# Kernel tuning notes

Measured on AMD Instinct MI355X. Metric: run time of the kernel, lower is better.

Reference implementation:

```python
import jax, jax.numpy as jnp
import numpy as np

NUM_NODES = 32768  # B*N = 16*2048
NUM_REL = 10
NUM_BASES = 4
D = 256
E = 524288


def _rgcn_layer(x, src, dst, rel, basis, comp, root, bias):
    """Basis-decomposed relational GCN layer with per-relation mean aggregation.
    x: [N, Din], basis: [NB, Din, Dout], comp: [R, NB], root: [Din, Dout], bias: [Dout].
    """
    n = x.shape[0]
    # project all nodes through each basis once: [N, NB, Dout]
    xb = jnp.einsum('ni,bio->nbo', x, basis)
    coeff = comp[rel]  # [E, NB] per-edge basis coefficients
    # mean normalization per (destination node, relation) pair
    seg = rel * n + dst  # combined segment id, [E]
    cnt = jax.ops.segment_sum(jnp.ones(rel.shape[0], x.dtype), seg,
                              num_segments=NUM_REL * n)
    inv = jnp.where(cnt > 0, 1.0 / cnt, 0.0)[seg]  # [E]
    # per-edge message: sum_b coeff[e,b] * xb[src_e, b, :] (loop over small NB)
    msg = jnp.zeros((rel.shape[0], basis.shape[2]), x.dtype)
    for b in range(basis.shape[0]):
        msg = msg + coeff[:, b:b + 1] * xb[src, b]
    msg = msg * inv[:, None]
    agg = jax.ops.segment_sum(msg, dst, num_segments=n)  # [N, Dout]
    return agg + x @ root + bias


def setup_inputs() -> dict:
    key = jax.random.key(0)
    ks = jax.random.split(key, 16)
    p = lambda k, shp: (jax.random.normal(k, shp, jnp.float32) * 0.05)
    inp = {
        'x': jax.random.normal(ks[0], (16, 2048, D), jnp.float32),
        't': jax.random.randint(ks[1], (16,), 0, 1000),
        'obj_cond': jax.random.randint(ks[2], (16, 2048), 0, 160),
        'edge_cond': jax.random.randint(ks[3], (2, E), 0, NUM_NODES),
        'relation_cond': jax.random.randint(ks[4], (E,), 0, NUM_REL),
        # layer 0: 256 -> 256 (hidden)
        'basis0': p(ks[5], (NUM_BASES, D, D)),
        'comp0': p(ks[6], (NUM_REL, NUM_BASES)),
        'root0': p(ks[7], (D, D)),
        'bias0': p(ks[8], (D,)),
        # layer 1: 256 -> 256 (output)
        'basis1': p(ks[9], (NUM_BASES, D, D)),
        'comp1': p(ks[10], (NUM_REL, NUM_BASES)),
        'root1': p(ks[11], (D, D)),
        'bias1': p(ks[12], (D,)),
    }
    return inp


def reference(x, t, obj_cond, edge_cond, relation_cond,
              basis0, comp0, root0, bias0, basis1, comp1, root1, bias1):
    B, N, Dm = x.shape
    h = x.reshape(B * N, Dm)
    src, dst = edge_cond[0], edge_cond[1]
    h = _rgcn_layer(h, src, dst, relation_cond, basis0, comp0, root0, bias0)
    h = jax.nn.relu(h)  # hidden-layer activation (dropout disabled at eval)
    h = _rgcn_layer(h, src, dst, relation_cond, basis1, comp1, root1, bias1)
    return h.reshape(B, N, Dm)
```

## Files before the change

kernel.cpp:

```cpp
#include <hip/hip_runtime.h>
#include <stdint.h>

#define NNODES 32768
#define NREL 10
#define NBASES 4
#define DIM 256
#define NEDGE 524288
#define KW 1280
#define KBASE 1024

#define HB 2048
#define CB 8192
#define WB 80

typedef __attribute__((ext_vector_type(8))) short bf16x8;
typedef __attribute__((ext_vector_type(4))) float f32x4;
typedef __attribute__((ext_vector_type(2))) float f32x2;

__device__ __forceinline__ float bf2f(unsigned short u){
  union { unsigned int i; float f; } v; v.i = ((unsigned int)u) << 16; return v.f;
}
__device__ __forceinline__ float asf(unsigned int u){
  union { unsigned int i; float f; } v; v.i = u; return v.f;
}
__device__ __forceinline__ unsigned short f2bf(float f){
  union { float f; unsigned int i; } v; v.f = f;
  unsigned int x = v.i;
  unsigned int r = (x + 0x7FFFu + ((x >> 16) & 1u)) >> 16;
  return (unsigned short)r;
}
__device__ __forceinline__ void gll16(const void* g, void* l){
  __builtin_amdgcn_global_load_lds((const __attribute__((address_space(1))) void*)g,
                                   (__attribute__((address_space(3))) void*)l, 16, 0, 0);
}

__global__ __launch_bounds__(256) void mega_prep(
    const int* __restrict__ ec, const int* __restrict__ rel,
    int* __restrict__ cnt_rd,
    const float* __restrict__ x, unsigned short* __restrict__ Xh,
    const float* __restrict__ basis0, const float* __restrict__ root0,
    unsigned short* __restrict__ Wt0,
    const float* __restrict__ basis1, const float* __restrict__ root1,
    unsigned short* __restrict__ Wt1)
{
  __shared__ float tile[64][65];
  int bid = blockIdx.x;
  int t = threadIdx.x;
  if (bid < HB){
    int e = bid * 256 + t;
    int d = ec[NEDGE + e];
    int r = rel[e];
    atomicAdd(&cnt_rd[(r << 15) + d], 1);
  } else if (bid < HB + CB){
    int i = (bid - HB) * 256 + t;
    float4 v = ((const float4*)x)[i];
    ushort4 o; o.x = f2bf(v.x); o.y = f2bf(v.y); o.z = f2bf(v.z); o.w = f2bf(v.w);
    ((ushort4*)Xh)[i] = o;
  } else {
    int b = bid - HB - CB;
    int layer = b / WB; b %= WB;
    const float* basis = layer ? basis1 : basis0;
    const float* root  = layer ? root1  : root0;
    unsigned short* Wt = layer ? Wt1    : Wt0;
    int k0 = (b % 20) * 64;
    int n0 = (b / 20) * 64;
    int tn = t & 63, tk = t >> 6;
#pragma unroll
    for (int i = 0; i < 64; i += 4){
      int k = k0 + tk + i;
      float v = (k < KBASE) ? basis[(size_t)k * 256 + n0 + tn]
                            : root[(size_t)(k - KBASE) * 256 + n0 + tn];
      tile[tk + i][tn] = v;
    }
    __syncthreads();
#pragma unroll
    for (int i = 0; i < 64; i += 4){
      int n = n0 + tk + i;
      Wt[(size_t)n * KW + k0 + tn] = f2bf(tile[tn][tk + i]);
    }
  }
}

__global__ __launch_bounds__(1024) void scan1(const int* __restrict__ cnt_rd,
                                              int* __restrict__ offs, int* __restrict__ blksum)
{
  __shared__ int sh[1024];
  int tid = threadIdx.x; int gid = blockIdx.x * 1024 + tid;
  int v = 0;
#pragma unroll
  for (int r = 0; r < NREL; r++) v += cnt_rd[(r << 15) + gid];
  sh[tid] = v; __syncthreads();
  for (int off = 1; off < 1024; off <<= 1){
    int t = (tid >= off) ? sh[tid - off] : 0;
    __syncthreads(); sh[tid] += t; __syncthreads();
  }
  offs[gid] = sh[tid] - v;
  if (tid == 1023) blksum[blockIdx.x] = sh[1023];
}
__global__ __launch_bounds__(1024) void scan3b(int* __restrict__ offs, const int* __restrict__ blksum)
{
  __shared__ int pre;
  int bid = blockIdx.x;
  if (threadIdx.x < 64){
    int v = ((int)threadIdx.x < bid && threadIdx.x < 32) ? blksum[threadIdx.x] : 0;
#pragma unroll
    for (int o = 1; o < 64; o <<= 1) v += __shfl_xor(v, o);
    if (threadIdx.x == 0) pre = v;
  }
  __syncthreads();
  int gid = bid * 1024 + threadIdx.x;
  offs[gid] += pre;
  if (gid == 0) offs[NNODES] = NEDGE;
}

__global__ void scatter_kernel(const int* __restrict__ ec, const int* __restrict__ rel,
                               const int* __restrict__ offs, int* __restrict__ cursor,
                               unsigned int* __restrict__ meta)
{
  int e = blockIdx.x * 256 + threadIdx.x;
  int s = ec[e];
  int d = ec[NEDGE + e];
  int r = rel[e];
  int p = offs[d] + atomicAdd(&cursor[d], 1);
  meta[p] = ((unsigned int)s << 4) | (unsigned int)r;
}

__global__ __launch_bounds__(256) void agg8(
    const unsigned short* __restrict__ Xin,
    const int* __restrict__ offs,
    const unsigned int* __restrict__ meta,
    const float* __restrict__ comp,
    const int* __restrict__ cnt_rd,
    unsigned short* __restrict__ z)
{
  __shared__ __attribute__((aligned(16))) float wtab[4][40];
  int t = threadIdx.x;
  int wv = t >> 6, lane = t & 63;
  int d = blockIdx.x * 4 + wv;
  if (lane < 40){
    int r = lane >> 2, b = lane & 3;
    int cnt = cnt_rd[(r << 15) + d];
    wtab[wv][lane] = (cnt > 0) ? comp[r * NBASES + b] / (float)cnt : 0.0f;
  }
  __syncthreads();

  const float4* wt4 = (const float4*)&wtab[wv][0];
  const char* Xb = (const char*)Xin;
  unsigned colb = (unsigned)(lane * 8);

  f32x2 acc[NBASES][2];
#pragma unroll
  for (int b = 0; b < NBASES; b++){ acc[b][0] = (f32x2){0.f,0.f}; acc[b][1] = (f32x2){0.f,0.f}; }

  int e0 = offs[d], e1 = offs[d + 1];
  int e = e0;

  for (; e + 7 < e1; e += 8){
    unsigned int m[8];
#pragma unroll
    for (int i = 0; i < 8; i++) m[i] = meta[e + i];
    uint2 v[8];
#pragma unroll
    for (int i = 0; i < 8; i++){
      unsigned off = ((m[i] & 0xFFFFFFF0u) << 5) + colb;
      v[i] = *(const uint2*)(Xb + off);
    }
#pragma unroll
    for (int i = 0; i < 8; i++){
      float4 w = wt4[m[i] & 15u];
      f32x2 f01, f23;
      f01.x = asf(v[i].x << 16); f01.y = asf(v[i].x & 0xffff0000u);
      f23.x = asf(v[i].y << 16); f23.y = asf(v[i].y & 0xffff0000u);
      acc[0][0] += (f32x2){w.x, w.x} * f01;  acc[0][1] += (f32x2){w.x, w.x} * f23;
      acc[1][0] += (f32x2){w.y, w.y} * f01;  acc[1][1] += (f32x2){w.y, w.y} * f23;
      acc[2][0] += (f32x2){w.z, w.z} * f01;  acc[2][1] += (f32x2){w.z, w.z} * f23;
      acc[3][0] += (f32x2){w.w, w.w} * f01;  acc[3][1] += (f32x2){w.w, w.w} * f23;
    }
  }

  for (; e < e1; e += 4){
    unsigned int m[4];
    float4 w[4];
#pragma unroll
    for (int i = 0; i < 4; i++){
      int ei = e + i;
      bool ok = ei < e1;
      m[i] = meta[ok ? ei : e1 - 1];
      float4 ww = wt4[m[i] & 15u];
      if (!ok){ ww.x = 0.f; ww.y = 0.f; ww.z = 0.f; ww.w = 0.f; }
      w[i] = ww;
    }
    uint2 v[4];
#pragma unroll
    for (int i = 0; i < 4; i++){
      unsigned off = ((m[i] & 0xFFFFFFF0u) << 5) + colb;
      v[i] = *(const uint2*)(Xb + off);
    }
#pragma unroll
    for (int i = 0; i < 4; i++){
      f32x2 f01, f23;
      f01.x = asf(v[i].x << 16); f01.y = asf(v[i].x & 0xffff0000u);
      f23.x = asf(v[i].y << 16); f23.y = asf(v[i].y & 0xffff0000u);
      acc[0][0] += (f32x2){w[i].x, w[i].x} * f01;  acc[0][1] += (f32x2){w[i].x, w[i].x} * f23;
      acc[1][0] += (f32x2){w[i].y, w[i].y} * f01;  acc[1][1] += (f32x2){w[i].y, w[i].y} * f23;
      acc[2][0] += (f32x2){w[i].z, w[i].z} * f01;  acc[2][1] += (f32x2){w[i].z, w[i].z} * f23;
      acc[3][0] += (f32x2){w[i].w, w[i].w} * f01;  acc[3][1] += (f32x2){w[i].w, w[i].w} * f23;
    }
  }

#pragma unroll
  for (int b = 0; b < NBASES; b++){
    ushort4 o;
    o.x = f2bf(acc[b][0].x); o.y = f2bf(acc[b][0].y);
    o.z = f2bf(acc[b][1].x); o.w = f2bf(acc[b][1].y);
    *(ushort4*)(z + (size_t)d * KBASE + b * 256 + lane * 4) = o;
  }
}

__global__ __launch_bounds__(256) void gemm8(
    const unsigned short* __restrict__ A0,
    const unsigned short* __restrict__ A1,
    const unsigned short* __restrict__ Wt,
    const float* __restrict__ bias,
    unsigned short* __restrict__ outh,
    float* __restrict__ outf,
    int mode)
{
  __shared__ __attribute__((aligned(16))) short As[64 * 64];
  int tid  = threadIdx.x;
  int m0   = blockIdx.x * 64;
  int lane = tid & 63;
  int wn   = tid >> 6;
  int lq = lane >> 4, lr = lane & 15;

  f32x4 zero = {0.f, 0.f, 0.f, 0.f};
  f32x4 acc[4][4];
#pragma unroll
  for (int i = 0; i < 4; i++)
#pragma unroll
    for (int j = 0; j < 4; j++) acc[i][j] = zero;

  int arow0 = tid >> 3;
  int akc0  = ((tid & 7) - (tid >> 4)) & 7;
  int g1    = tid + 256;
  int arow1 = g1 >> 3;
  int akc1  = ((g1 & 7) - (g1 >> 4)) & 7;

  const unsigned short* wtb[4];
#pragma unroll
  for (int j = 0; j < 4; j++)
    wtb[j] = Wt + (size_t)(wn * 64 + j * 16 + lr) * KW + lq * 8;

  for (int k0 = 0; k0 < KW; k0 += 64){
    __syncthreads();
    {
      const unsigned short* ga0, *ga1;
      if (k0 < KBASE){
        ga0 = A0 + (size_t)(m0 + arow0) * KBASE + k0 + akc0 * 8;
        ga1 = A0 + (size_t)(m0 + arow1) * KBASE + k0 + akc1 * 8;
      } else {
        ga0 = A1 + (size_t)(m0 + arow0) * 256 + (k0 - KBASE) + akc0 * 8;
        ga1 = A1 + (size_t)(m0 + arow1) * 256 + (k0 - KBASE) + akc1 * 8;
      }
      gll16(ga0, As + tid * 8);
      gll16(ga1, As + (tid + 256) * 8);
    }
    bf16x8 bfr[4][2];
#pragma unroll
    for (int j = 0; j < 4; j++)
#pragma unroll
      for (int s = 0; s < 2; s++)
        bfr[j][s] = *(const bf16x8*)(wtb[j] + k0 + s * 32);
    __syncthreads();

    bf16x8 af[4][2];
#pragma unroll
    for (int i = 0; i < 4; i++){
      int row = i * 16 + lr;
#pragma unroll
      for (int s = 0; s < 2; s++){
        int slot = ((lq + 4 * s) + (row >> 1)) & 7;
        af[i][s] = *(const bf16x8*)(As + row * 64 + slot * 8);
      }
    }
#pragma unroll
    for (int i = 0; i < 4; i++)
#pragma unroll
      for (int j = 0; j < 4; j++){
        acc[i][j] = __builtin_amdgcn_mfma_f32_16x16x32_bf16(af[i][0], bfr[j][0], acc[i][j], 0, 0, 0);
        acc[i][j] = __builtin_amdgcn_mfma_f32_16x16x32_bf16(af[i][1], bfr[j][1], acc[i][j], 0, 0, 0);
      }
  }

#pragma unroll
  for (int i = 0; i < 4; i++)
#pragma unroll
    for (int j = 0; j < 4; j++)
#pragma unroll
      for (int r = 0; r < 4; r++){
        int gm = m0 + i * 16 + lq * 4 + r;
        int gn = wn * 64 + j * 16 + lr;
        float v = acc[i][j][r] + bias[gn];
        size_t idx = (size_t)gm * 256 + gn;
        if (mode == 1) outh[idx] = f2bf(fmaxf(v, 0.f));
        else           outf[idx] = v;
      }
}

extern "C" void kernel_launch(void* const* d_in, const int* in_sizes, int n_in,
                              void* d_out, int out_size, void* d_ws, size_t ws_size,
                              hipStream_t stream)
{
  const float* x      = (const float*)d_in[0];
  const int*   ec     = (const int*)d_in[3];
  const int*   rel    = (const int*)d_in[4];
  const float* basis0 = (const float*)d_in[5];
  const float* comp0  = (const float*)d_in[6];
  const float* root0  = (const float*)d_in[7];
  const float* bias0  = (const float*)d_in[8];
  const float* basis1 = (const float*)d_in[9];
  const float* comp1  = (const float*)d_in[10];
  const float* root1  = (const float*)d_in[11];
  const float* bias1  = (const float*)d_in[12];

  char* p = (char*)d_ws;
  unsigned short* z   = (unsigned short*)p; p += (size_t)NNODES * KBASE * 2;
  unsigned short* Xh  = (unsigned short*)p; p += (size_t)NNODES * DIM * 2;
  unsigned short* h   = (unsigned short*)p; p += (size_t)NNODES * DIM * 2;
  unsigned short* Wt0 = (unsigned short*)p; p += (size_t)256 * KW * 2;
  unsigned short* Wt1 = (unsigned short*)p; p += (size_t)256 * KW * 2;
  unsigned int* meta  = (unsigned int*)p;   p += (size_t)NEDGE * 4;
  int* cnt_rd  = (int*)p;   p += (size_t)NREL * NNODES * 4;
  int* cursor  = (int*)p;   p += (size_t)NNODES * 4;
  int* offs    = (int*)p;   p += (size_t)(NNODES + 1) * 4;
  int* blksum  = (int*)p;   p += 1024;

  hipMemsetAsync(cnt_rd, 0, ((size_t)NREL * NNODES + (size_t)NNODES) * 4, stream);

  mega_prep<<<HB + CB + 2 * WB, 256, 0, stream>>>(
      ec, rel, cnt_rd, x, Xh, basis0, root0, Wt0, basis1, root1, Wt1);

  scan1<<<NNODES / 1024, 1024, 0, stream>>>(cnt_rd, offs, blksum);
  scan3b<<<NNODES / 1024, 1024, 0, stream>>>(offs, blksum);
  scatter_kernel<<<NEDGE / 256, 256, 0, stream>>>(ec, rel, offs, cursor, meta);

  agg8<<<NNODES / 4, 256, 0, stream>>>(Xh, offs, meta, comp0, cnt_rd, z);
  gemm8<<<NNODES / 64, 256, 0, stream>>>(z, Xh, Wt0, bias0, h, nullptr, 1);

  agg8<<<NNODES / 4, 256, 0, stream>>>(h, offs, meta, comp1, cnt_rd, z);
  gemm8<<<NNODES / 64, 256, 0, stream>>>(z, h, Wt1, bias1, nullptr, (float*)d_out, 2);
}
```

Measured before the change: 352.0 us.

## Retile GEMM to 128x128 with LDS-staged weights; simplify scan and CSR scatter

The GEMM moves from 64-row tiles that read weights straight from global into registers to 128x128 output tiles. Both A and B are staged in LDS with 32-wide K steps and a 2x2 wave layout, which raises data reuse per block. The scan now uses wavefront shuffles instead of a barrier-heavy shared-memory Hillis-Steele loop. The scatter step increments the offsets array in place, so the separate cursor buffer and part of the memset are gone, and the aggregation reads [offs[d-1], offs[d]). The tradeoffs are fewer blocks (512), twice as many K iterations with barriers, and offsets that now rely on in-place atomics.

```diff
diff --git a/kernel.cpp b/kernel.cpp
--- a/kernel.cpp
+++ b/kernel.cpp
@@ -84,18 +84,33 @@
 __global__ __launch_bounds__(1024) void scan1(const int* __restrict__ cnt_rd,
                                               int* __restrict__ offs, int* __restrict__ blksum)
 {
-  __shared__ int sh[1024];
+  __shared__ int wsum[16];
   int tid = threadIdx.x; int gid = blockIdx.x * 1024 + tid;
+  int lane = tid & 63, wv = tid >> 6;
   int v = 0;
 #pragma unroll
   for (int r = 0; r < NREL; r++) v += cnt_rd[(r << 15) + gid];
-  sh[tid] = v; __syncthreads();
-  for (int off = 1; off < 1024; off <<= 1){
-    int t = (tid >= off) ? sh[tid - off] : 0;
-    __syncthreads(); sh[tid] += t; __syncthreads();
-  }
-  offs[gid] = sh[tid] - v;
-  if (tid == 1023) blksum[blockIdx.x] = sh[1023];
+  int incl = v;
+#pragma unroll
+  for (int o = 1; o < 64; o <<= 1){
+    int t = __shfl_up(incl, o);
+    if (lane >= o) incl += t;
+  }
+  if (lane == 63) wsum[wv] = incl;
+  __syncthreads();
+  if (wv == 0){
+    int s = (lane < 16) ? wsum[lane] : 0;
+#pragma unroll
+    for (int o = 1; o < 16; o <<= 1){
+      int t = __shfl_up(s, o);
+      if (lane >= o) s += t;
+    }
+    if (lane < 16) wsum[lane] = s;
+  }
+  __syncthreads();
+  int base = wv ? wsum[wv - 1] : 0;
+  offs[gid] = base + incl - v;
+  if (tid == 1023) blksum[blockIdx.x] = base + incl;
 }
 __global__ __launch_bounds__(1024) void scan3b(int* __restrict__ offs, const int* __restrict__ blksum)
 {
@@ -110,18 +125,17 @@
   __syncthreads();
   int gid = bid * 1024 + threadIdx.x;
   offs[gid] += pre;
-  if (gid == 0) offs[NNODES] = NEDGE;
 }
 
 __global__ void scatter_kernel(const int* __restrict__ ec, const int* __restrict__ rel,
-                               const int* __restrict__ offs, int* __restrict__ cursor,
+                               int* __restrict__ offs,
                                unsigned int* __restrict__ meta)
 {
   int e = blockIdx.x * 256 + threadIdx.x;
   int s = ec[e];
   int d = ec[NEDGE + e];
   int r = rel[e];
-  int p = offs[d] + atomicAdd(&cursor[d], 1);
+  int p = atomicAdd(&offs[d], 1);
   meta[p] = ((unsigned int)s << 4) | (unsigned int)r;
 }
 
@@ -152,7 +166,8 @@
 #pragma unroll
   for (int b = 0; b < NBASES; b++){ acc[b][0] = (f32x2){0.f,0.f}; acc[b][1] = (f32x2){0.f,0.f}; }
 
-  int e0 = offs[d], e1 = offs[d + 1];
+  int e1 = offs[d];
+  int e0 = (d == 0) ? 0 : offs[d - 1];
   int e = e0;
 
   for (; e + 7 < e1; e += 8){
@@ -217,7 +232,7 @@
   }
 }
 
-__global__ __launch_bounds__(256) void gemm8(
+__global__ __launch_bounds__(256) void gemm9(
     const unsigned short* __restrict__ A0,
     const unsigned short* __restrict__ A1,
     const unsigned short* __restrict__ Wt,
@@ -226,11 +241,15 @@
     float* __restrict__ outf,
     int mode)
 {
-  __shared__ __attribute__((aligned(16))) short As[64 * 64];
+  __shared__ __attribute__((aligned(16))) short As[128 * 32];
+  __shared__ __attribute__((aligned(16))) short Bs[128 * 32];
   int tid  = threadIdx.x;
-  int m0   = blockIdx.x * 64;
+  int bid  = blockIdx.x;
+  int m0   = (bid >> 1) * 128;
+  int n0   = (bid & 1) * 128;
   int lane = tid & 63;
-  int wn   = tid >> 6;
+  int w    = tid >> 6;
+  int wm   = w >> 1, wn = w & 1;
   int lq = lane >> 4, lr = lane & 15;
 
   f32x4 zero = {0.f, 0.f, 0.f, 0.f};
@@ -240,66 +259,54 @@
 #pragma unroll
     for (int j = 0; j < 4; j++) acc[i][j] = zero;
 
-  int arow0 = tid >> 3;
-  int akc0  = ((tid & 7) - (tid >> 4)) & 7;
-  int g1    = tid + 256;
-  int arow1 = g1 >> 3;
-  int akc1  = ((g1 & 7) - (g1 >> 4)) & 7;
-
-  const unsigned short* wtb[4];
-#pragma unroll
-  for (int j = 0; j < 4; j++)
-    wtb[j] = Wt + (size_t)(wn * 64 + j * 16 + lr) * KW + lq * 8;
-
-  for (int k0 = 0; k0 < KW; k0 += 64){
+  int g1   = tid + 256;
+  int ar0  = tid >> 2, ak0 = ((tid & 3) - (tid >> 3)) & 3;
+  int ar1  = g1 >> 2,  ak1 = ((g1 & 3) - (g1 >> 3)) & 3;
+
+  for (int k0 = 0; k0 < KW; k0 += 32){
     __syncthreads();
     {
-      const unsigned short* ga0, *ga1;
+      const unsigned short *ga0, *ga1;
       if (k0 < KBASE){
-        ga0 = A0 + (size_t)(m0 + arow0) * KBASE + k0 + akc0 * 8;
-        ga1 = A0 + (size_t)(m0 + arow1) * KBASE + k0 + akc1 * 8;
+        ga0 = A0 + (size_t)(m0 + ar0) * KBASE + k0 + ak0 * 8;
+        ga1 = A0 + (size_t)(m0 + ar1) * KBASE + k0 + ak1 * 8;
       } else {
-        ga0 = A1 + (size_t)(m0 + arow0) * 256 + (k0 - KBASE) + akc0 * 8;
-        ga1 = A1 + (size_t)(m0 + arow1) * 256 + (k0 - KBASE) + akc1 * 8;
+        ga0 = A1 + (size_t)(m0 + ar0) * 256 + (k0 - KBASE) + ak0 * 8;
+        ga1 = A1 + (size_t)(m0 + ar1) * 256 + (k0 - KBASE) + ak1 * 8;
       }
       gll16(ga0, As + tid * 8);
-      gll16(ga1, As + (tid + 256) * 8);
-    }
-    bf16x8 bfr[4][2];
+      gll16(ga1, As + g1 * 8);
+      gll16(Wt + (size_t)(n0 + ar0) * KW + k0 + ak0 * 8, Bs + tid * 8);
+      gll16(Wt + (size_t)(n0 + ar1) * KW + k0 + ak1 * 8, Bs + g1 * 8);
+    }
+    __syncthreads();
+
+    bf16x8 af[4], bfr[4];
+#pragma unroll
+    for (int i = 0; i < 4; i++){
+      int row = wm * 64 + i * 16 + lr;
+      af[i] = *(const bf16x8*)(As + row * 32 + (((lq + (row >> 1)) & 3) * 8));
+    }
+#pragma unroll
+    for (int j = 0; j < 4; j++){
+      int row = wn * 64 + j * 16 + lr;
+      bfr[j] = *(const bf16x8*)(Bs + row * 32 + (((lq + (row >> 1)) & 3) * 8));
+    }
+#pragma unroll
+    for (int i = 0; i < 4; i++)
+#pragma unroll
+      for (int j = 0; j < 4; j++)
+        acc[i][j] = __builtin_amdgcn_mfma_f32_16x16x32_bf16(af[i], bfr[j], acc[i][j], 0, 0, 0);
+  }
+
+#pragma unroll
+  for (int i = 0; i < 4; i++)
 #pragma unroll
     for (int j = 0; j < 4; j++)
 #pragma unroll
-      for (int s = 0; s < 2; s++)
-        bfr[j][s] = *(const bf16x8*)(wtb[j] + k0 + s * 32);
-    __syncthreads();
-
-    bf16x8 af[4][2];
-#pragma unroll
-    for (int i = 0; i < 4; i++){
-      int row = i * 16 + lr;
-#pragma unroll
-      for (int s = 0; s < 2; s++){
-        int slot = ((lq + 4 * s) + (row >> 1)) & 7;
-        af[i][s] = *(const bf16x8*)(As + row * 64 + slot * 8);
-      }
-    }
-#pragma unroll
-    for (int i = 0; i < 4; i++)
-#pragma unroll
-      for (int j = 0; j < 4; j++){
-        acc[i][j] = __builtin_amdgcn_mfma_f32_16x16x32_bf16(af[i][0], bfr[j][0], acc[i][j], 0, 0, 0);
-        acc[i][j] = __builtin_amdgcn_mfma_f32_16x16x32_bf16(af[i][1], bfr[j][1], acc[i][j], 0, 0, 0);
-      }
-  }
-
-#pragma unroll
-  for (int i = 0; i < 4; i++)
-#pragma unroll
-    for (int j = 0; j < 4; j++)
-#pragma unroll
       for (int r = 0; r < 4; r++){
-        int gm = m0 + i * 16 + lq * 4 + r;
-        int gn = wn * 64 + j * 16 + lr;
+        int gm = m0 + wm * 64 + i * 16 + lq * 4 + r;
+        int gn = n0 + wn * 64 + j * 16 + lr;
         float v = acc[i][j][r] + bias[gn];
         size_t idx = (size_t)gm * 256 + gn;
         if (mode == 1) outh[idx] = f2bf(fmaxf(v, 0.f));
@@ -331,22 +338,21 @@
   unsigned short* Wt1 = (unsigned short*)p; p += (size_t)256 * KW * 2;
   unsigned int* meta  = (unsigned int*)p;   p += (size_t)NEDGE * 4;
   int* cnt_rd  = (int*)p;   p += (size_t)NREL * NNODES * 4;
-  int* cursor  = (int*)p;   p += (size_t)NNODES * 4;
   int* offs    = (int*)p;   p += (size_t)(NNODES + 1) * 4;
   int* blksum  = (int*)p;   p += 1024;
 
-  hipMemsetAsync(cnt_rd, 0, ((size_t)NREL * NNODES + (size_t)NNODES) * 4, stream);
+  hipMemsetAsync(cnt_rd, 0, (size_t)NREL * NNODES * 4, stream);
 
   mega_prep<<<HB + CB + 2 * WB, 256, 0, stream>>>(
       ec, rel, cnt_rd, x, Xh, basis0, root0, Wt0, basis1, root1, Wt1);
 
   scan1<<<NNODES / 1024, 1024, 0, stream>>>(cnt_rd, offs, blksum);
   scan3b<<<NNODES / 1024, 1024, 0, stream>>>(offs, blksum);
-  scatter_kernel<<<NEDGE / 256, 256, 0, stream>>>(ec, rel, offs, cursor, meta);
+  scatter_kernel<<<NEDGE / 256, 256, 0, stream>>>(ec, rel, offs, meta);
 
   agg8<<<NNODES / 4, 256, 0, stream>>>(Xh, offs, meta, comp0, cnt_rd, z);
-  gemm8<<<NNODES / 64, 256, 0, stream>>>(z, Xh, Wt0, bias0, h, nullptr, 1);
+  gemm9<<<(NNODES / 128) * 2, 256, 0, stream>>>(z, Xh, Wt0, bias0, h, nullptr, 1);
 
   agg8<<<NNODES / 4, 256, 0, stream>>>(h, offs, meta, comp1, cnt_rd, z);
-  gemm8<<<NNODES / 64, 256, 0, stream>>>(z, h, Wt1, bias1, nullptr, (float*)d_out, 2);
-}
+  gemm9<<<(NNODES / 128) * 2, 256, 0, stream>>>(z, h, Wt1, bias1, nullptr, (float*)d_out, 2);
+}
```

Result: faster. 322.3 us (median of 2 runs) (-8.4%).
